# Optimization experiments

Hardware: AMD Instinct MI355X
Metric: run time of the kernel (lower is better)

## Reference

```python
import jax, jax.numpy as jnp
import numpy as np

NUM_USERS = 50000
NUM_ITEMS = 100000
N = NUM_USERS + NUM_ITEMS
D = 64
K = 3
E = 1000000


def setup_inputs() -> dict:
    key = jax.random.key(0)
    k1, k2, k3, k4 = jax.random.split(key, 4)
    users_emb = jax.random.normal(k1, (NUM_USERS, D), dtype=jnp.float32)
    items_emb = jax.random.normal(k2, (NUM_ITEMS, D), dtype=jnp.float32)
    src = jax.random.randint(k3, (E,), 0, N, dtype=jnp.int32)
    dst = jax.random.randint(k4, (E,), 0, N, dtype=jnp.int32)
    return {"users_emb": users_emb, "items_emb": items_emb, "src": src, "dst": dst}


def reference(users_emb, items_emb, src, dst):
    all_emb = jnp.concatenate([users_emb, items_emb], axis=0)  # [N, D]
    # out_degrees: number of outgoing edges per node, clamped to >= 1
    deg = jax.ops.segment_sum(jnp.ones((E,), dtype=jnp.float32), src, num_segments=N)
    normed_deg = jnp.power(jnp.clip(deg, 1.0, None), -0.5)[:, None]  # [N, 1]

    def conv(emb):
        h = emb * normed_deg                                  # D^{-1/2} * x
        agg = jax.ops.segment_sum(h[src], dst, num_segments=N)  # copy_u + sum
        return agg * normed_deg                               # * D^{-1/2}

    acc = all_emb
    emb = all_emb
    for _ in range(K):
        emb = conv(emb)
        acc = acc + emb
    final = acc / (K + 1)  # mean over layer embeddings
    return final[:NUM_USERS], final[NUM_USERS:]
```

## Files before the change

### kernel.cpp

```cpp
#include <hip/hip_runtime.h>

#define NUSERS 50000
#define NITEMS 100000
#define NNODES 150000
#define DIM 64
#define BSTRIDE 32

static __device__ __forceinline__ float bf2f(unsigned short u) {
    return __uint_as_float(((unsigned)u) << 16);
}
static __device__ __forceinline__ unsigned short f2bf(float f) {
    unsigned u = __float_as_uint(f);
    return (unsigned short)((u + 0x7fffu + ((u >> 16) & 1u)) >> 16);
}
static __device__ __forceinline__ float4 cvt4(ushort4 u) {
    return make_float4(bf2f(u.x), bf2f(u.y), bf2f(u.z), bf2f(u.w));
}
static __device__ __forceinline__ ushort4 pack4(float4 v) {
    return make_ushort4(f2bf(v.x), f2bf(v.y), f2bf(v.z), f2bf(v.w));
}

__global__ void hist_place_kernel(const int* __restrict__ src,
                                  const int* __restrict__ dst,
                                  int* __restrict__ outdeg,
                                  int* __restrict__ indeg,
                                  int* __restrict__ csr, int E) {
    int e = blockIdx.x * blockDim.x + threadIdx.x;
    if (e >= E) return;
    int s = src[e];
    int d = dst[e];
    atomicAdd(&outdeg[s], 1);
    int r = atomicAdd(&indeg[d], 1);
    if (r < BSTRIDE) csr[d * BSTRIDE + r] = s;
}

__global__ void prescale_kernel(const float4* __restrict__ users4,
                                const float4* __restrict__ items4,
                                const int* __restrict__ outdeg,
                                ushort4* __restrict__ s0) {
    int t = blockIdx.x * blockDim.x + threadIdx.x;
    int v = t >> 4;
    int l = t & 15;
    if (v >= NNODES) return;
    float ns = rsqrtf(fmaxf((float)outdeg[v], 1.0f));
    float4 r = (v < NUSERS) ? users4[v * 16 + l] : items4[(v - NUSERS) * 16 + l];
    r.x *= ns; r.y *= ns; r.z *= ns; r.w *= ns;
    s0[v * 16 + l] = pack4(r);
}

__global__ void gather_mid_kernel(const int* __restrict__ csr,
                                  const int* __restrict__ indeg,
                                  const int* __restrict__ outdeg,
                                  const ushort4* __restrict__ cur,
                                  ushort4* __restrict__ nxt) {
    int t = blockIdx.x * blockDim.x + threadIdx.x;
    int v = t >> 4;
    int l = t & 15;
    if (v >= NNODES) return;
    int start = v * BSTRIDE;
    int cnt = min(indeg[v], BSTRIDE);
    float4 sum = make_float4(0.f, 0.f, 0.f, 0.f);
#pragma unroll 4
    for (int k = 0; k < cnt; ++k) {
        int s = csr[start + k];
        float4 r = cvt4(cur[s * 16 + l]);
        sum.x += r.x; sum.y += r.y; sum.z += r.z; sum.w += r.w;
    }
    float inv_d = 1.0f / fmaxf((float)outdeg[v], 1.0f);
    sum.x *= inv_d; sum.y *= inv_d; sum.z *= inv_d; sum.w *= inv_d;
    nxt[v * 16 + l] = pack4(sum);
}

__global__ void gather_last_kernel(const int* __restrict__ csr,
                                   const int* __restrict__ indeg,
                                   const int* __restrict__ outdeg,
                                   const ushort4* __restrict__ s2,
                                   const ushort4* __restrict__ s1,
                                   const float4* __restrict__ users4,
                                   const float4* __restrict__ items4,
                                   float4* __restrict__ out4) {
    int t = blockIdx.x * blockDim.x + threadIdx.x;
    int v = t >> 4;
    int l = t & 15;
    if (v >= NNODES) return;
    int start = v * BSTRIDE;
    int cnt = min(indeg[v], BSTRIDE);
    float4 sum = make_float4(0.f, 0.f, 0.f, 0.f);
#pragma unroll 4
    for (int k = 0; k < cnt; ++k) {
        int s = csr[start + k];
        float4 r = cvt4(s2[s * 16 + l]);
        sum.x += r.x; sum.y += r.y; sum.z += r.z; sum.w += r.w;
    }
    float d  = fmaxf((float)outdeg[v], 1.0f);
    float ns = rsqrtf(d);
    float sq = d * ns;
    int o = v * 16 + l;
    float4 orig = (v < NUSERS) ? users4[o] : items4[(v - NUSERS) * 16 + l];
    float4 a1 = cvt4(s1[o]);
    float4 a2 = cvt4(s2[o]);
    float4 r;
    r.x = (orig.x + (a1.x + a2.x) * sq + sum.x * ns) * 0.25f;
    r.y = (orig.y + (a1.y + a2.y) * sq + sum.y * ns) * 0.25f;
    r.z = (orig.z + (a1.z + a2.z) * sq + sum.z * ns) * 0.25f;
    r.w = (orig.w + (a1.w + a2.w) * sq + sum.w * ns) * 0.25f;
    out4[o] = r;
}

extern "C" void kernel_launch(void* const* d_in, const int* in_sizes, int n_in,
                              void* d_out, int out_size, void* d_ws, size_t ws_size,
                              hipStream_t stream) {
    const int* src = (const int*)d_in[2];
    const int* dst = (const int*)d_in[3];
    const int  E   = in_sizes[2];
    const float4* users4 = (const float4*)d_in[0];
    const float4* items4 = (const float4*)d_in[1];
    float4* out4 = (float4*)d_out;

    char* w = (char*)d_ws;
    int*     outdeg = (int*)w;    w += sizeof(int) * NNODES;
    int*     indeg  = (int*)w;    w += sizeof(int) * NNODES;
    int*     csr    = (int*)w;    w += sizeof(int) * (size_t)NNODES * BSTRIDE;
    ushort4* s0     = (ushort4*)w; w += sizeof(unsigned short) * (size_t)NNODES * DIM;
    ushort4* s1     = (ushort4*)w; w += sizeof(unsigned short) * (size_t)NNODES * DIM;
    ushort4* s2     = (ushort4*)w;

    const int BLK  = 256;
    const int gedg = (E + BLK - 1) / BLK;
    const int ggat = (NNODES * 16 + BLK - 1) / BLK;

    hipMemsetAsync(outdeg, 0, sizeof(int) * NNODES * 2, stream);
    hist_place_kernel<<<gedg, BLK, 0, stream>>>(src, dst, outdeg, indeg, csr, E);
    prescale_kernel<<<ggat, BLK, 0, stream>>>(users4, items4, outdeg, s0);

    gather_mid_kernel<<<ggat, BLK, 0, stream>>>(csr, indeg, outdeg, s0, s1);
    gather_mid_kernel<<<ggat, BLK, 0, stream>>>(csr, indeg, outdeg, s1, s2);
    gather_last_kernel<<<ggat, BLK, 0, stream>>>(csr, indeg, outdeg, s2, s1,
                                                 users4, items4, out4);
}
```

Measured before the change: 213.1 us.

## Use one wavefront per node with split-neighbor gather and vectorized edge/prescale loads

Gather kernels now assign a full 64-lane wavefront per destination node. The neighbor list is loaded once into lanes and broadcast with shuffles, and the two half-waves each process alternate neighbors on packed bf16 pairs before a cross-half reduction. The histogram kernel handles two edges per thread via int2 loads, and prescale writes 16-byte packed rows. The aim is to replace per-lane redundant CSR index loads and expose more memory-level parallelism, at the cost of 4x more threads and idle lanes when degree is small.

```diff
diff --git a/kernel.cpp b/kernel.cpp
--- a/kernel.cpp
+++ b/kernel.cpp
@@ -6,105 +6,129 @@
 #define DIM 64
 #define BSTRIDE 32
 
-static __device__ __forceinline__ float bf2f(unsigned short u) {
-    return __uint_as_float(((unsigned)u) << 16);
-}
 static __device__ __forceinline__ unsigned short f2bf(float f) {
     unsigned u = __float_as_uint(f);
     return (unsigned short)((u + 0x7fffu + ((u >> 16) & 1u)) >> 16);
 }
-static __device__ __forceinline__ float4 cvt4(ushort4 u) {
-    return make_float4(bf2f(u.x), bf2f(u.y), bf2f(u.z), bf2f(u.w));
-}
-static __device__ __forceinline__ ushort4 pack4(float4 v) {
-    return make_ushort4(f2bf(v.x), f2bf(v.y), f2bf(v.z), f2bf(v.w));
+static __device__ __forceinline__ unsigned pack2(float lo, float hi) {
+    return (unsigned)f2bf(lo) | ((unsigned)f2bf(hi) << 16);
 }
 
-__global__ void hist_place_kernel(const int* __restrict__ src,
-                                  const int* __restrict__ dst,
+__global__ void hist_place_kernel(const int2* __restrict__ src2,
+                                  const int2* __restrict__ dst2,
                                   int* __restrict__ outdeg,
                                   int* __restrict__ indeg,
-                                  int* __restrict__ csr, int E) {
-    int e = blockIdx.x * blockDim.x + threadIdx.x;
-    if (e >= E) return;
-    int s = src[e];
-    int d = dst[e];
-    atomicAdd(&outdeg[s], 1);
-    int r = atomicAdd(&indeg[d], 1);
-    if (r < BSTRIDE) csr[d * BSTRIDE + r] = s;
+                                  int* __restrict__ csr, int E2) {
+    int i = blockIdx.x * blockDim.x + threadIdx.x;
+    if (i >= E2) return;
+    int2 s = src2[i];
+    int2 d = dst2[i];
+    atomicAdd(&outdeg[s.x], 1);
+    atomicAdd(&outdeg[s.y], 1);
+    int r0 = atomicAdd(&indeg[d.x], 1);
+    int r1 = atomicAdd(&indeg[d.y], 1);
+    if (r0 < BSTRIDE) csr[d.x * BSTRIDE + r0] = s.x;
+    if (r1 < BSTRIDE) csr[d.y * BSTRIDE + r1] = s.y;
 }
 
 __global__ void prescale_kernel(const float4* __restrict__ users4,
                                 const float4* __restrict__ items4,
                                 const int* __restrict__ outdeg,
-                                ushort4* __restrict__ s0) {
+                                uint4* __restrict__ s0) {
     int t = blockIdx.x * blockDim.x + threadIdx.x;
-    int v = t >> 4;
-    int l = t & 15;
+    int v = t >> 3;
+    int l = t & 7;
     if (v >= NNODES) return;
     float ns = rsqrtf(fmaxf((float)outdeg[v], 1.0f));
-    float4 r = (v < NUSERS) ? users4[v * 16 + l] : items4[(v - NUSERS) * 16 + l];
-    r.x *= ns; r.y *= ns; r.z *= ns; r.w *= ns;
-    s0[v * 16 + l] = pack4(r);
+    const float4* rowp = (v < NUSERS) ? users4 + (size_t)v * 16
+                                      : items4 + (size_t)(v - NUSERS) * 16;
+    float4 a = rowp[l * 2];
+    float4 b = rowp[l * 2 + 1];
+    uint4 p;
+    p.x = pack2(a.x * ns, a.y * ns);
+    p.y = pack2(a.z * ns, a.w * ns);
+    p.z = pack2(b.x * ns, b.y * ns);
+    p.w = pack2(b.z * ns, b.w * ns);
+    s0[(size_t)v * 8 + l] = p;
 }
 
-__global__ void gather_mid_kernel(const int* __restrict__ csr,
-                                  const int* __restrict__ indeg,
-                                  const int* __restrict__ outdeg,
-                                  const ushort4* __restrict__ cur,
-                                  ushort4* __restrict__ nxt) {
-    int t = blockIdx.x * blockDim.x + threadIdx.x;
-    int v = t >> 4;
-    int l = t & 15;
-    if (v >= NNODES) return;
-    int start = v * BSTRIDE;
-    int cnt = min(indeg[v], BSTRIDE);
-    float4 sum = make_float4(0.f, 0.f, 0.f, 0.f);
+__global__ void gather_mid_w(const int* __restrict__ csr,
+                             const int* __restrict__ indeg,
+                             const int* __restrict__ outdeg,
+                             const unsigned* __restrict__ cur,
+                             unsigned* __restrict__ nxt) {
+    int wid = (blockIdx.x * blockDim.x + threadIdx.x) >> 6;
+    int lane = threadIdx.x & 63;
+    if (wid >= NNODES) return;
+    int v = wid;
+    int cnt  = min(indeg[v], BSTRIDE);
+    int half = lane >> 5;
+    int dh   = lane & 31;
+    int s_ent = csr[v * BSTRIDE + dh];
+    float slo = 0.f, shi = 0.f;
 #pragma unroll 4
-    for (int k = 0; k < cnt; ++k) {
-        int s = csr[start + k];
-        float4 r = cvt4(cur[s * 16 + l]);
-        sum.x += r.x; sum.y += r.y; sum.z += r.z; sum.w += r.w;
+    for (int k = 0; k < cnt; k += 2) {
+        int slot = k + half;
+        int s = __shfl(s_ent, slot);
+        if (slot < cnt) {
+            unsigned u = cur[(size_t)s * 32 + dh];
+            slo += __uint_as_float(u << 16);
+            shi += __uint_as_float(u & 0xffff0000u);
+        }
     }
-    float inv_d = 1.0f / fmaxf((float)outdeg[v], 1.0f);
-    sum.x *= inv_d; sum.y *= inv_d; sum.z *= inv_d; sum.w *= inv_d;
-    nxt[v * 16 + l] = pack4(sum);
+    slo += __shfl_xor(slo, 32);
+    shi += __shfl_xor(shi, 32);
+    if (lane < 32) {
+        float inv_d = 1.0f / fmaxf((float)outdeg[v], 1.0f);
+        nxt[(size_t)v * 32 + dh] = pack2(slo * inv_d, shi * inv_d);
+    }
 }
 
-__global__ void gather_last_kernel(const int* __restrict__ csr,
-                                   const int* __restrict__ indeg,
-                                   const int* __restrict__ outdeg,
-                                   const ushort4* __restrict__ s2,
-                                   const ushort4* __restrict__ s1,
-                                   const float4* __restrict__ users4,
-                                   const float4* __restrict__ items4,
-                                   float4* __restrict__ out4) {
-    int t = blockIdx.x * blockDim.x + threadIdx.x;
-    int v = t >> 4;
-    int l = t & 15;
-    if (v >= NNODES) return;
-    int start = v * BSTRIDE;
-    int cnt = min(indeg[v], BSTRIDE);
-    float4 sum = make_float4(0.f, 0.f, 0.f, 0.f);
+__global__ void gather_last_w(const int* __restrict__ csr,
+                              const int* __restrict__ indeg,
+                              const int* __restrict__ outdeg,
+                              const unsigned* __restrict__ s2,
+                              const unsigned* __restrict__ s1,
+                              const float2* __restrict__ users2,
+                              const float2* __restrict__ items2,
+                              float2* __restrict__ out2) {
+    int wid = (blockIdx.x * blockDim.x + threadIdx.x) >> 6;
+    int lane = threadIdx.x & 63;
+    if (wid >= NNODES) return;
+    int v = wid;
+    int cnt  = min(indeg[v], BSTRIDE);
+    int half = lane >> 5;
+    int dh   = lane & 31;
+    int s_ent = csr[v * BSTRIDE + dh];
+    float slo = 0.f, shi = 0.f;
 #pragma unroll 4
-    for (int k = 0; k < cnt; ++k) {
-        int s = csr[start + k];
-        float4 r = cvt4(s2[s * 16 + l]);
-        sum.x += r.x; sum.y += r.y; sum.z += r.z; sum.w += r.w;
+    for (int k = 0; k < cnt; k += 2) {
+        int slot = k + half;
+        int s = __shfl(s_ent, slot);
+        if (slot < cnt) {
+            unsigned u = s2[(size_t)s * 32 + dh];
+            slo += __uint_as_float(u << 16);
+            shi += __uint_as_float(u & 0xffff0000u);
+        }
     }
-    float d  = fmaxf((float)outdeg[v], 1.0f);
-    float ns = rsqrtf(d);
-    float sq = d * ns;
-    int o = v * 16 + l;
-    float4 orig = (v < NUSERS) ? users4[o] : items4[(v - NUSERS) * 16 + l];
-    float4 a1 = cvt4(s1[o]);
-    float4 a2 = cvt4(s2[o]);
-    float4 r;
-    r.x = (orig.x + (a1.x + a2.x) * sq + sum.x * ns) * 0.25f;
-    r.y = (orig.y + (a1.y + a2.y) * sq + sum.y * ns) * 0.25f;
-    r.z = (orig.z + (a1.z + a2.z) * sq + sum.z * ns) * 0.25f;
-    r.w = (orig.w + (a1.w + a2.w) * sq + sum.w * ns) * 0.25f;
-    out4[o] = r;
+    slo += __shfl_xor(slo, 32);
+    shi += __shfl_xor(shi, 32);
+    if (lane < 32) {
+        float d  = fmaxf((float)outdeg[v], 1.0f);
+        float ns = rsqrtf(d);
+        float sq = d * ns;
+        size_t o = (size_t)v * 32 + dh;
+        float2 orig = (v < NUSERS) ? users2[o]
+                                   : items2[(size_t)(v - NUSERS) * 32 + dh];
+        unsigned u1 = s1[o];
+        unsigned u2 = s2[o];
+        float alo = __uint_as_float(u1 << 16)         + __uint_as_float(u2 << 16);
+        float ahi = __uint_as_float(u1 & 0xffff0000u) + __uint_as_float(u2 & 0xffff0000u);
+        float2 r;
+        r.x = (orig.x + alo * sq + slo * ns) * 0.25f;
+        r.y = (orig.y + ahi * sq + shi * ns) * 0.25f;
+        out2[o] = r;
+    }
 }
 
 extern "C" void kernel_launch(void* const* d_in, const int* in_sizes, int n_in,
@@ -115,26 +139,29 @@
     const int  E   = in_sizes[2];
     const float4* users4 = (const float4*)d_in[0];
     const float4* items4 = (const float4*)d_in[1];
-    float4* out4 = (float4*)d_out;
 
     char* w = (char*)d_ws;
-    int*     outdeg = (int*)w;    w += sizeof(int) * NNODES;
-    int*     indeg  = (int*)w;    w += sizeof(int) * NNODES;
-    int*     csr    = (int*)w;    w += sizeof(int) * (size_t)NNODES * BSTRIDE;
-    ushort4* s0     = (ushort4*)w; w += sizeof(unsigned short) * (size_t)NNODES * DIM;
-    ushort4* s1     = (ushort4*)w; w += sizeof(unsigned short) * (size_t)NNODES * DIM;
-    ushort4* s2     = (ushort4*)w;
+    int*      outdeg = (int*)w;      w += sizeof(int) * NNODES;
+    int*      indeg  = (int*)w;      w += sizeof(int) * NNODES;
+    int*      csr    = (int*)w;      w += sizeof(int) * (size_t)NNODES * BSTRIDE;
+    unsigned* s0     = (unsigned*)w; w += sizeof(unsigned short) * (size_t)NNODES * DIM;
+    unsigned* s1     = (unsigned*)w; w += sizeof(unsigned short) * (size_t)NNODES * DIM;
+    unsigned* s2     = (unsigned*)w;
 
-    const int BLK  = 256;
-    const int gedg = (E + BLK - 1) / BLK;
-    const int ggat = (NNODES * 16 + BLK - 1) / BLK;
+    const int E2    = E / 2;
+    const int ghst  = (E2 + 127) / 128;
+    const int gpre  = (NNODES * 8 + 255) / 256;
+    const int gwav  = (NNODES * 64 + 255) / 256;
 
     hipMemsetAsync(outdeg, 0, sizeof(int) * NNODES * 2, stream);
-    hist_place_kernel<<<gedg, BLK, 0, stream>>>(src, dst, outdeg, indeg, csr, E);
-    prescale_kernel<<<ggat, BLK, 0, stream>>>(users4, items4, outdeg, s0);
+    hist_place_kernel<<<ghst, 128, 0, stream>>>((const int2*)src, (const int2*)dst,
+                                                outdeg, indeg, csr, E2);
+    prescale_kernel<<<gpre, 256, 0, stream>>>(users4, items4, outdeg, (uint4*)s0);
 
-    gather_mid_kernel<<<ggat, BLK, 0, stream>>>(csr, indeg, outdeg, s0, s1);
-    gather_mid_kernel<<<ggat, BLK, 0, stream>>>(csr, indeg, outdeg, s1, s2);
-    gather_last_kernel<<<ggat, BLK, 0, stream>>>(csr, indeg, outdeg, s2, s1,
-                                                 users4, items4, out4);
+    gather_mid_w<<<gwav, 256, 0, stream>>>(csr, indeg, outdeg, s0, s1);
+    gather_mid_w<<<gwav, 256, 0, stream>>>(csr, indeg, outdeg, s1, s2);
+    gather_last_w<<<gwav, 256, 0, stream>>>(csr, indeg, outdeg, s2, s1,
+                                            (const float2*)users4,
+                                            (const float2*)items4,
+                                            (float2*)d_out);
 }
```

Measured after the change: 295.7 us. 1.39x slower.
